# Kernel tuning notes

Measured on AMD Instinct MI355X. Metric: run time of the kernel, lower is better.

Reference implementation:

```python
import jax, jax.numpy as jnp
import numpy as np
import math

HIDDEN_DIM = 1024
NUM_HEAD = 16
HEAD_DIM = HIDDEN_DIM // NUM_HEAD


def setup_inputs() -> dict:
    key = jax.random.key(0)
    ks = jax.random.split(key, 9)
    B, S, D = 2, 2048, HIDDEN_DIM
    scale = 1.0 / math.sqrt(D)
    x = jax.random.normal(ks[0], (B, S, D), dtype=jnp.float32)
    wq = jax.random.normal(ks[1], (D, D), dtype=jnp.float32) * scale
    bq = jnp.zeros((D,), dtype=jnp.float32)
    wk = jax.random.normal(ks[2], (D, D), dtype=jnp.float32) * scale
    bk = jnp.zeros((D,), dtype=jnp.float32)
    wv = jax.random.normal(ks[3], (D, D), dtype=jnp.float32) * scale
    bv = jnp.zeros((D,), dtype=jnp.float32)
    wo = jax.random.normal(ks[4], (D, D), dtype=jnp.float32) * scale
    bo = jnp.zeros((D,), dtype=jnp.float32)
    return {"x": x, "wq": wq, "bq": bq, "wk": wk, "bk": bk,
            "wv": wv, "bv": bv, "wo": wo, "bo": bo}


def reference(x, wq, bq, wk, bk, wv, bv, wo, bo):
    B, S, D = x.shape
    H, Hd = NUM_HEAD, HEAD_DIM
    # QKV projections (torch Linear: y = x @ W^T + b)
    q = (x @ wq.T + bq).reshape(B, S, H, Hd).transpose(0, 2, 1, 3)  # [B,H,S,Hd]
    k = (x @ wk.T + bk).reshape(B, S, H, Hd).transpose(0, 2, 1, 3)
    v = (x @ wv.T + bv).reshape(B, S, H, Hd).transpose(0, 2, 1, 3)
    logits = jnp.einsum('bhsd,bhtd->bhst', q, k) / jnp.sqrt(jnp.float32(Hd))
    scores = jax.nn.softmax(logits, axis=-1)  # [B,H,S,S]
    out = jnp.einsum('bhst,bhtd->bhsd', scores, v)
    out = out.transpose(0, 2, 1, 3).reshape(B, S, D)
    return out @ wo.T + bo
```

## Files before the change

kernel.cpp:

```cpp
#include <hip/hip_runtime.h>
#include <hip/hip_bf16.h>
#include <math.h>

#define DEV __device__ __forceinline__

typedef float f32x4 __attribute__((ext_vector_type(4)));
typedef float f32x16 __attribute__((ext_vector_type(16)));
typedef __bf16 b16x8 __attribute__((ext_vector_type(8)));
typedef unsigned short ushort_t;
typedef ushort_t u16x8 __attribute__((ext_vector_type(8)));

#define BATCH 2
#define SEQ 2048
#define DMODEL 1024
#define NHEAD 16
#define HDIM 64
#define MROWS (BATCH * SEQ)
#define LOG2E 1.44269504088896f

#define OFF_XB   ((size_t)0)
#define OFF_WB   ((size_t)4 * 1024 * 1024)
#define OFF_WOB  ((size_t)7 * 1024 * 1024)
#define OFF_QKV  ((size_t)8 * 1024 * 1024)
#define OFF_OB   ((size_t)20 * 1024 * 1024)

DEV ushort_t f2bf(float f) {
    union { float f; unsigned u; } v; v.f = f;
    unsigned r = v.u + 0x7fffu + ((v.u >> 16) & 1u);
    return (ushort_t)(r >> 16);
}

DEV unsigned cvt_pk_bf16(float lo, float hi) {
    unsigned r;
    asm("v_cvt_pk_bf16_f32 %0, %1, %2" : "=v"(r) : "v"(lo), "v"(hi));
    return r;
}

DEV void permswap(unsigned &a, unsigned &b) {
    asm("v_permlane32_swap_b32 %0, %1" : "+v"(a), "+v"(b));
}

DEV f32x4 mfma16(u16x8 a, u16x8 b, f32x4 c) {
    return __builtin_amdgcn_mfma_f32_16x16x32_bf16(
        __builtin_bit_cast(b16x8, a), __builtin_bit_cast(b16x8, b), c, 0, 0, 0);
}

DEV f32x16 mfma32(u16x8 a, u16x8 b, f32x16 c) {
    return __builtin_amdgcn_mfma_f32_32x32x16_bf16(
        __builtin_bit_cast(b16x8, a), __builtin_bit_cast(b16x8, b), c, 0, 0, 0);
}

DEV void gload_lds16(const ushort_t* g, ushort_t* l) {
    __builtin_amdgcn_global_load_lds(
        (const __attribute__((address_space(1))) unsigned int*)g,
        (__attribute__((address_space(3))) unsigned int*)l, 16, 0, 0);
}

__global__ __launch_bounds__(256) void convert5(
    const float* __restrict__ x, const float* __restrict__ wq,
    const float* __restrict__ wk, const float* __restrict__ wv,
    const float* __restrict__ wo,
    ushort_t* __restrict__ xb, ushort_t* __restrict__ wb, ushort_t* __restrict__ wob)
{
    const int ai = blockIdx.y;
    const float* src; ushort_t* dst; int n;
    if (ai == 0)      { src = x;  dst = xb;                 n = MROWS * DMODEL; }
    else if (ai == 1) { src = wq; dst = wb;                 n = DMODEL * DMODEL; }
    else if (ai == 2) { src = wk; dst = wb + 1024 * 1024;   n = DMODEL * DMODEL; }
    else if (ai == 3) { src = wv; dst = wb + 2 * 1024 * 1024; n = DMODEL * DMODEL; }
    else              { src = wo; dst = wob;                n = DMODEL * DMODEL; }
    int idx = (blockIdx.x * 256 + threadIdx.x) * 4;
    int stride = gridDim.x * 256 * 4;
    for (int i = idx; i < n; i += stride) {
        float4 f = *(const float4*)(src + i);
        ushort4 u;
        u.x = f2bf(f.x); u.y = f2bf(f.y); u.z = f2bf(f.z); u.w = f2bf(f.w);
        *(ushort4*)(dst + i) = u;
    }
}

#define SWZ(row, col) ((col) ^ (((row) & 7) << 3))
template<int MODE>
__global__ __launch_bounds__(256) void gemm_nt(
    const ushort_t* __restrict__ A,
    const ushort_t* __restrict__ W,
    const float* __restrict__ b0, const float* __restrict__ b1, const float* __restrict__ b2,
    ushort_t* __restrict__ obf,
    float* __restrict__ of32)
{
    __shared__ __attribute__((aligned(16))) ushort_t ldsA[128 * 64];
    __shared__ __attribute__((aligned(16))) ushort_t ldsB[128 * 64];

    const int t = threadIdx.x;
    const int m0 = blockIdx.x * 128;
    const int n0 = blockIdx.y * 128;
    const int mat = blockIdx.z;
    const ushort_t* Wm = W + (size_t)mat * (1024 * 1024);
    const float* bias = (mat == 0) ? b0 : (mat == 1 ? b1 : b2);

    const int lane = t & 63, wave = t >> 6;
    const int wr = (wave >> 1) * 64, wc = (wave & 1) * 64;
    const int lr = lane & 15, lk = (lane >> 4) * 8;

    f32x4 acc[4][4] = {};

    for (int k0 = 0; k0 < DMODEL; k0 += 64) {
#pragma unroll
        for (int i = 0; i < 4; ++i) {
            int e = (i * 256 + t) * 8;
            int row = e >> 6, col = e & 63;
            gload_lds16(A  + (size_t)(m0 + row) * DMODEL + k0 + SWZ(row, col), &ldsA[e]);
            gload_lds16(Wm + (size_t)(n0 + row) * DMODEL + k0 + SWZ(row, col), &ldsB[e]);
        }
        __syncthreads();
#pragma unroll
        for (int kk = 0; kk < 2; ++kk) {
            u16x8 av[4], bv[4];
#pragma unroll
            for (int i = 0; i < 4; ++i) {
                int ar = wr + i * 16 + lr;
                av[i] = *(const u16x8*)&ldsA[ar * 64 + SWZ(ar, kk * 32 + lk)];
            }
#pragma unroll
            for (int i = 0; i < 4; ++i) {
                int br = wc + i * 16 + lr;
                bv[i] = *(const u16x8*)&ldsB[br * 64 + SWZ(br, kk * 32 + lk)];
            }
#pragma unroll
            for (int m = 0; m < 4; ++m)
#pragma unroll
                for (int n = 0; n < 4; ++n)
                    acc[m][n] = mfma16(av[m], bv[n], acc[m][n]);
        }
        __syncthreads();
    }

    const int lgr = (lane >> 4) * 4;
    if (MODE == 0) {
        ushort_t* dst = obf + (size_t)mat * ((size_t)MROWS * DMODEL);
        if (mat < 2) {
            const float qscale = (mat == 0) ? (0.125f * LOG2E) : 1.0f;
#pragma unroll
            for (int m = 0; m < 4; ++m) {
                int row = m0 + wr + m * 16 + lgr;
#pragma unroll
                for (int n = 0; n < 4; ++n) {
                    int col = n0 + wc + n * 16 + lr;
                    float bcol = bias[col];
                    int h = col >> 6, hd = col & 63;
#pragma unroll
                    for (int r = 0; r < 4; ++r) {
                        int rr = row + r;
                        int bb = rr >> 11, s = rr & 2047;
                        float v = (acc[m][n][r] + bcol) * qscale;
                        dst[(((size_t)bb * NHEAD + h) * SEQ + s) * HDIM + hd] = f2bf(v);
                    }
                }
            }
        } else {
#pragma unroll
            for (int m = 0; m < 4; ++m) {
                int row = m0 + wr + m * 16 + lgr;
                int bb = row >> 11, s = row & 2047;
#pragma unroll
                for (int n = 0; n < 4; ++n) {
                    int col = n0 + wc + n * 16 + lr;
                    float bcol = bias[col];
                    int h = col >> 6, hd = col & 63;
                    ushort4 pk;
                    pk.x = f2bf(acc[m][n][0] + bcol);
                    pk.y = f2bf(acc[m][n][1] + bcol);
                    pk.z = f2bf(acc[m][n][2] + bcol);
                    pk.w = f2bf(acc[m][n][3] + bcol);
                    *(ushort4*)&dst[(((size_t)bb * NHEAD + h) * HDIM + hd) * SEQ + s] = pk;
                }
            }
        }
    } else {
#pragma unroll
        for (int m = 0; m < 4; ++m) {
            int row = m0 + wr + m * 16 + lgr;
#pragma unroll
            for (int n = 0; n < 4; ++n) {
                int col = n0 + wc + n * 16 + lr;
                float bcol = b0[col];
#pragma unroll
                for (int r = 0; r < 4; ++r)
                    of32[(size_t)(row + r) * DMODEL + col] = acc[m][n][r] + bcol;
            }
        }
    }
}

__global__ __launch_bounds__(256, 2) void attn(
    const ushort_t* __restrict__ Q, const ushort_t* __restrict__ K,
    const ushort_t* __restrict__ Vt, ushort_t* __restrict__ O)
{
    __shared__ __attribute__((aligned(16))) ushort_t kt[128 * 72];
    __shared__ __attribute__((aligned(16))) ushort_t vt[64 * 136];
    __shared__ float abuf[4][32];

    const int t = threadIdx.x, lane = t & 63, wave = t >> 6;
    const int lq = lane & 31, hi = lane >> 5;

    const int id = blockIdx.x;
    const int swz = (id & 7) * 64 + (id >> 3);
    const int q0 = (swz & 15) * 128;
    const int h = (swz >> 4) & 15, b = swz >> 8;

    const size_t base = ((size_t)(b * NHEAD + h)) * (SEQ * HDIM);
    const ushort_t* Qh = Q + base;
    const ushort_t* Kh = K + base;
    const ushort_t* Vh = Vt + base;

    const int q0w = q0 + wave * 32;

    u16x8 qf[4];
#pragma unroll
    for (int step = 0; step < 4; ++step)
        qf[step] = *(const u16x8*)(Qh + (size_t)(q0w + lq) * HDIM + step * 16 + hi * 8);

    f32x16 o0 = {}, o1 = {};
    float m_run = 0.f, l_run = 0.f;

    const int krow = t >> 1, kc = (t & 1) * 32;
    const int vrow = t >> 2, vc = (t & 3) * 32;

    for (int t0 = 0; t0 < SEQ; t0 += 128) {
        {
            const ushort_t* kg = Kh + (size_t)(t0 + krow) * HDIM + kc;
            u16x8 ka = *(const u16x8*)kg;
            u16x8 kb = *(const u16x8*)(kg + 8);
            u16x8 kc2 = *(const u16x8*)(kg + 16);
            u16x8 kd = *(const u16x8*)(kg + 24);
            ushort_t* kl = &kt[krow * 72 + kc];
            *(u16x8*)(kl)      = ka;
            *(u16x8*)(kl + 8)  = kb;
            *(u16x8*)(kl + 16) = kc2;
            *(u16x8*)(kl + 24) = kd;
            const ushort_t* vg = Vh + (size_t)vrow * SEQ + t0 + vc;
            u16x8 va = *(const u16x8*)vg;
            u16x8 vb = *(const u16x8*)(vg + 8);
            u16x8 vc2 = *(const u16x8*)(vg + 16);
            u16x8 vd = *(const u16x8*)(vg + 24);
            ushort_t* vl = &vt[vrow * 136 + vc];
            *(u16x8*)(vl)      = va;
            *(u16x8*)(vl + 8)  = vb;
            *(u16x8*)(vl + 16) = vc2;
            *(u16x8*)(vl + 24) = vd;
        }
        __syncthreads();

        f32x16 sv[4];
#pragma unroll
        for (int n = 0; n < 4; ++n)
#pragma unroll
            for (int r = 0; r < 16; ++r) sv[n][r] = -m_run;
#pragma unroll
        for (int step = 0; step < 4; ++step) {
#pragma unroll
            for (int n = 0; n < 4; ++n) {
                u16x8 kf = *(const u16x8*)&kt[(n * 32 + lq) * 72 + step * 16 + hi * 8];
                sv[n] = mfma32(kf, qf[step], sv[n]);
            }
        }

        f32x16 mm;
#pragma unroll
        for (int r = 0; r < 16; ++r)
            mm[r] = fmaxf(fmaxf(sv[0][r], sv[1][r]), fmaxf(sv[2][r], sv[3][r]));
        float h8[8];
#pragma unroll
        for (int k = 0; k < 8; ++k) h8[k] = fmaxf(mm[k], mm[k + 8]);
        float h4[4];
#pragma unroll
        for (int k = 0; k < 4; ++k) h4[k] = fmaxf(h8[k], h8[k + 4]);
        float pm = fmaxf(fmaxf(h4[0], h4[1]), fmaxf(h4[2], h4[3]));
        pm = fmaxf(pm, __shfl_xor(pm, 32));

        if (__any(pm > 8.0f)) {
            float dlt = fmaxf(pm, 0.f);
            float alpha = __builtin_amdgcn_exp2f(-dlt);
            m_run += dlt;
#pragma unroll
            for (int n = 0; n < 4; ++n)
#pragma unroll
                for (int r = 0; r < 16; ++r)
                    sv[n][r] = __builtin_amdgcn_exp2f(sv[n][r] - dlt);
            if (lane < 32) abuf[wave][lq] = alpha;
#pragma unroll
            for (int g = 0; g < 4; ++g) {
                f32x4 a4 = *(const f32x4*)&abuf[wave][g * 8 + hi * 4];
#pragma unroll
                for (int k = 0; k < 4; ++k) {
                    o0[g * 4 + k] *= a4[k];
                    o1[g * 4 + k] *= a4[k];
                }
            }
            l_run *= alpha;
        } else {
#pragma unroll
            for (int n = 0; n < 4; ++n)
#pragma unroll
                for (int r = 0; r < 16; ++r)
                    sv[n][r] = __builtin_amdgcn_exp2f(sv[n][r]);
        }

        f32x16 ss;
#pragma unroll
        for (int r = 0; r < 16; ++r)
            ss[r] = (sv[0][r] + sv[1][r]) + (sv[2][r] + sv[3][r]);
        float s8[8];
#pragma unroll
        for (int k = 0; k < 8; ++k) s8[k] = ss[k] + ss[k + 8];
        float s4[4];
#pragma unroll
        for (int k = 0; k < 4; ++k) s4[k] = s8[k] + s8[k + 4];
        float ps = (s4[0] + s4[1]) + (s4[2] + s4[3]);
        ps += __shfl_xor(ps, 32);
        l_run += ps;

#pragma unroll
        for (int s = 0; s < 8; ++s) {
            const int n = s >> 1, g0 = (s & 1) * 2;
            unsigned xA = cvt_pk_bf16(sv[n][4 * g0 + 0], sv[n][4 * g0 + 1]);
            unsigned yA = cvt_pk_bf16(sv[n][4 * g0 + 2], sv[n][4 * g0 + 3]);
            unsigned xB = cvt_pk_bf16(sv[n][4 * g0 + 4], sv[n][4 * g0 + 5]);
            unsigned yB = cvt_pk_bf16(sv[n][4 * g0 + 6], sv[n][4 * g0 + 7]);
            permswap(xA, xB);
            permswap(yA, yB);
            uint4 w4; w4.x = xA; w4.y = yA; w4.z = xB; w4.w = yB;
            u16x8 pa = __builtin_bit_cast(u16x8, w4);
            u16x8 vf0 = *(const u16x8*)&vt[(lq)      * 136 + s * 16 + hi * 8];
            u16x8 vf1 = *(const u16x8*)&vt[(32 + lq) * 136 + s * 16 + hi * 8];
            o0 = mfma32(pa, vf0, o0);
            o1 = mfma32(pa, vf1, o1);
        }
        __syncthreads();
    }

    float linv = 1.0f / l_run;
    if (lane < 32) abuf[wave][lq] = linv;
#pragma unroll
    for (int g = 0; g < 4; ++g) {
        f32x4 l4 = *(const f32x4*)&abuf[wave][g * 8 + hi * 4];
#pragma unroll
        for (int k = 0; k < 4; ++k) {
            int r = g * 4 + k;
            int sg = q0w + g * 8 + hi * 4 + k;
            size_t obase = ((size_t)(b * SEQ + sg)) * DMODEL + h * HDIM;
            O[obase + lq]      = f2bf(o0[r] * l4[k]);
            O[obase + 32 + lq] = f2bf(o1[r] * l4[k]);
        }
    }
}

extern "C" void kernel_launch(void* const* d_in, const int* in_sizes, int n_in,
                              void* d_out, int out_size, void* d_ws, size_t ws_size,
                              hipStream_t stream) {
    const float* x  = (const float*)d_in[0];
    const float* wq = (const float*)d_in[1];
    const float* bq = (const float*)d_in[2];
    const float* wk = (const float*)d_in[3];
    const float* bk = (const float*)d_in[4];
    const float* wv = (const float*)d_in[5];
    const float* bv = (const float*)d_in[6];
    const float* wo = (const float*)d_in[7];
    const float* bo = (const float*)d_in[8];
    float* out = (float*)d_out;

    ushort_t* ws  = (ushort_t*)d_ws;
    ushort_t* xb  = ws + OFF_XB;
    ushort_t* wb  = ws + OFF_WB;
    ushort_t* wob = ws + OFF_WOB;
    ushort_t* qkv = ws + OFF_QKV;
    ushort_t* Qb  = qkv;
    ushort_t* Kb  = qkv + (size_t)4 * 1024 * 1024;
    ushort_t* Vb  = qkv + (size_t)8 * 1024 * 1024;
    ushort_t* Ob  = ws + OFF_OB;

    convert5<<<dim3(1024, 5, 1), 256, 0, stream>>>(x, wq, wk, wv, wo, xb, wb, wob);
    gemm_nt<0><<<dim3(32, 8, 3), 256, 0, stream>>>(xb, wb, bq, bk, bv, qkv, nullptr);
    attn<<<dim3(512, 1, 1), 256, 0, stream>>>(Qb, Kb, Vb, Ob);
    gemm_nt<1><<<dim3(32, 8, 1), 256, 0, stream>>>(Ob, wob, bo, nullptr, nullptr, nullptr, out);
}
```

Measured before the change: 124.6 us.

## Shrink attention blocks to 2 waves and KV tiles to 64 keys

Result: slower. 245.6 us (+97.1%).

```diff
diff --git a/kernel.cpp b/kernel.cpp
--- a/kernel.cpp
+++ b/kernel.cpp
@@ -192,21 +192,21 @@
     }
 }
 
-__global__ __launch_bounds__(256, 2) void attn(
+__global__ __launch_bounds__(128, 4) void attn(
     const ushort_t* __restrict__ Q, const ushort_t* __restrict__ K,
     const ushort_t* __restrict__ Vt, ushort_t* __restrict__ O)
 {
-    __shared__ __attribute__((aligned(16))) ushort_t kt[128 * 72];
-    __shared__ __attribute__((aligned(16))) ushort_t vt[64 * 136];
-    __shared__ float abuf[4][32];
+    __shared__ __attribute__((aligned(16))) ushort_t kt[64 * 72];
+    __shared__ __attribute__((aligned(16))) ushort_t vt[64 * 72];
+    __shared__ float abuf[2][32];
 
     const int t = threadIdx.x, lane = t & 63, wave = t >> 6;
     const int lq = lane & 31, hi = lane >> 5;
 
     const int id = blockIdx.x;
-    const int swz = (id & 7) * 64 + (id >> 3);
-    const int q0 = (swz & 15) * 128;
-    const int h = (swz >> 4) & 15, b = swz >> 8;
+    const int swz = (id & 7) * 128 + (id >> 3);
+    const int q0 = (swz & 31) * 64;
+    const int h = (swz >> 5) & 15, b = swz >> 9;
 
     const size_t base = ((size_t)(b * NHEAD + h)) * (SEQ * HDIM);
     const ushort_t* Qh = Q + base;
@@ -223,27 +223,27 @@
     f32x16 o0 = {}, o1 = {};
     float m_run = 0.f, l_run = 0.f;
 
-    const int krow = t >> 1, kc = (t & 1) * 32;
-    const int vrow = t >> 2, vc = (t & 3) * 32;
-
-    for (int t0 = 0; t0 < SEQ; t0 += 128) {
+    const int srow = t >> 1;
+    const int sc0 = (t & 1) * 32;
+
+    for (int t0 = 0; t0 < SEQ; t0 += 64) {
         {
-            const ushort_t* kg = Kh + (size_t)(t0 + krow) * HDIM + kc;
+            const ushort_t* kg = Kh + (size_t)(t0 + srow) * HDIM + sc0;
             u16x8 ka = *(const u16x8*)kg;
             u16x8 kb = *(const u16x8*)(kg + 8);
             u16x8 kc2 = *(const u16x8*)(kg + 16);
             u16x8 kd = *(const u16x8*)(kg + 24);
-            ushort_t* kl = &kt[krow * 72 + kc];
+            ushort_t* kl = &kt[srow * 72 + sc0];
             *(u16x8*)(kl)      = ka;
             *(u16x8*)(kl + 8)  = kb;
             *(u16x8*)(kl + 16) = kc2;
             *(u16x8*)(kl + 24) = kd;
-            const ushort_t* vg = Vh + (size_t)vrow * SEQ + t0 + vc;
+            const ushort_t* vg = Vh + (size_t)srow * SEQ + t0 + sc0;
             u16x8 va = *(const u16x8*)vg;
             u16x8 vb = *(const u16x8*)(vg + 8);
             u16x8 vc2 = *(const u16x8*)(vg + 16);
             u16x8 vd = *(const u16x8*)(vg + 24);
-            ushort_t* vl = &vt[vrow * 136 + vc];
+            ushort_t* vl = &vt[srow * 72 + sc0];
             *(u16x8*)(vl)      = va;
             *(u16x8*)(vl + 8)  = vb;
             *(u16x8*)(vl + 16) = vc2;
@@ -251,24 +251,20 @@
         }
         __syncthreads();
 
-        f32x16 sv[4];
-#pragma unroll
-        for (int n = 0; n < 4; ++n)
-#pragma unroll
-            for (int r = 0; r < 16; ++r) sv[n][r] = -m_run;
+        f32x16 s0, s1;
+#pragma unroll
+        for (int r = 0; r < 16; ++r) { s0[r] = -m_run; s1[r] = -m_run; }
 #pragma unroll
         for (int step = 0; step < 4; ++step) {
-#pragma unroll
-            for (int n = 0; n < 4; ++n) {
-                u16x8 kf = *(const u16x8*)&kt[(n * 32 + lq) * 72 + step * 16 + hi * 8];
-                sv[n] = mfma32(kf, qf[step], sv[n]);
-            }
+            u16x8 kf0 = *(const u16x8*)&kt[(lq)      * 72 + step * 16 + hi * 8];
+            u16x8 kf1 = *(const u16x8*)&kt[(32 + lq) * 72 + step * 16 + hi * 8];
+            s0 = mfma32(kf0, qf[step], s0);
+            s1 = mfma32(kf1, qf[step], s1);
         }
 
         f32x16 mm;
 #pragma unroll
-        for (int r = 0; r < 16; ++r)
-            mm[r] = fmaxf(fmaxf(sv[0][r], sv[1][r]), fmaxf(sv[2][r], sv[3][r]));
+        for (int r = 0; r < 16; ++r) mm[r] = fmaxf(s0[r], s1[r]);
         float h8[8];
 #pragma unroll
         for (int k = 0; k < 8; ++k) h8[k] = fmaxf(mm[k], mm[k + 8]);
@@ -283,10 +279,10 @@
             float alpha = __builtin_amdgcn_exp2f(-dlt);
             m_run += dlt;
 #pragma unroll
-            for (int n = 0; n < 4; ++n)
-#pragma unroll
-                for (int r = 0; r < 16; ++r)
-                    sv[n][r] = __builtin_amdgcn_exp2f(sv[n][r] - dlt);
+            for (int r = 0; r < 16; ++r) {
+                s0[r] = __builtin_amdgcn_exp2f(s0[r] - dlt);
+                s1[r] = __builtin_amdgcn_exp2f(s1[r] - dlt);
+            }
             if (lane < 32) abuf[wave][lq] = alpha;
 #pragma unroll
             for (int g = 0; g < 4; ++g) {
@@ -300,16 +296,15 @@
             l_run *= alpha;
         } else {
 #pragma unroll
-            for (int n = 0; n < 4; ++n)
-#pragma unroll
-                for (int r = 0; r < 16; ++r)
-                    sv[n][r] = __builtin_amdgcn_exp2f(sv[n][r]);
+            for (int r = 0; r < 16; ++r) {
+                s0[r] = __builtin_amdgcn_exp2f(s0[r]);
+                s1[r] = __builtin_amdgcn_exp2f(s1[r]);
+            }
         }
 
         f32x16 ss;
 #pragma unroll
-        for (int r = 0; r < 16; ++r)
-            ss[r] = (sv[0][r] + sv[1][r]) + (sv[2][r] + sv[3][r]);
+        for (int r = 0; r < 16; ++r) ss[r] = s0[r] + s1[r];
         float s8[8];
 #pragma unroll
         for (int k = 0; k < 8; ++k) s8[k] = ss[k] + ss[k + 8];
@@ -321,18 +316,26 @@
         l_run += ps;
 
 #pragma unroll
-        for (int s = 0; s < 8; ++s) {
-            const int n = s >> 1, g0 = (s & 1) * 2;
-            unsigned xA = cvt_pk_bf16(sv[n][4 * g0 + 0], sv[n][4 * g0 + 1]);
-            unsigned yA = cvt_pk_bf16(sv[n][4 * g0 + 2], sv[n][4 * g0 + 3]);
-            unsigned xB = cvt_pk_bf16(sv[n][4 * g0 + 4], sv[n][4 * g0 + 5]);
-            unsigned yB = cvt_pk_bf16(sv[n][4 * g0 + 6], sv[n][4 * g0 + 7]);
+        for (int s = 0; s < 4; ++s) {
+            const int g0 = (s & 1) * 2;
+            unsigned xA, yA, xB, yB;
+            if (s < 2) {
+                xA = cvt_pk_bf16(s0[4 * g0 + 0], s0[4 * g0 + 1]);
+                yA = cvt_pk_bf16(s0[4 * g0 + 2], s0[4 * g0 + 3]);
+                xB = cvt_pk_bf16(s0[4 * g0 + 4], s0[4 * g0 + 5]);
+                yB = cvt_pk_bf16(s0[4 * g0 + 6], s0[4 * g0 + 7]);
+            } else {
+                xA = cvt_pk_bf16(s1[4 * g0 + 0], s1[4 * g0 + 1]);
+                yA = cvt_pk_bf16(s1[4 * g0 + 2], s1[4 * g0 + 3]);
+                xB = cvt_pk_bf16(s1[4 * g0 + 4], s1[4 * g0 + 5]);
+                yB = cvt_pk_bf16(s1[4 * g0 + 6], s1[4 * g0 + 7]);
+            }
             permswap(xA, xB);
             permswap(yA, yB);
             uint4 w4; w4.x = xA; w4.y = yA; w4.z = xB; w4.w = yB;
             u16x8 pa = __builtin_bit_cast(u16x8, w4);
-            u16x8 vf0 = *(const u16x8*)&vt[(lq)      * 136 + s * 16 + hi * 8];
-            u16x8 vf1 = *(const u16x8*)&vt[(32 + lq) * 136 + s * 16 + hi * 8];
+            u16x8 vf0 = *(const u16x8*)&vt[(lq)      * 72 + s * 16 + hi * 8];
+            u16x8 vf1 = *(const u16x8*)&vt[(32 + lq) * 72 + s * 16 + hi * 8];
             o0 = mfma32(pa, vf0, o0);
             o1 = mfma32(pa, vf1, o1);
         }
@@ -381,6 +384,6 @@
 
     convert5<<<dim3(1024, 5, 1), 256, 0, stream>>>(x, wq, wk, wv, wo, xb, wb, wob);
     gemm_nt<0><<<dim3(32, 8, 3), 256, 0, stream>>>(xb, wb, bq, bk, bv, qkv, nullptr);
-    attn<<<dim3(512, 1, 1), 256, 0, stream>>>(Qb, Kb, Vb, Ob);
+    attn<<<dim3(1024, 1, 1), 128, 0, stream>>>(Qb, Kb, Vb, Ob);
     gemm_nt<1><<<dim3(32, 8, 1), 256, 0, stream>>>(Ob, wob, bo, nullptr, nullptr, nullptr, out);
 }
```
